# Kernel optimization log

Measured on AMD Instinct MI355X. Metric: run time of the kernel, lower is better.

The kernel has to match this reference:

```python
import jax, jax.numpy as jnp
import numpy as np

B, T, D = 8, 4096, 256
GATE_MIN, GATE_MAX = 0.01, 0.99


def setup_inputs() -> dict:
    key = jax.random.key(0)
    ks = jax.random.split(key, 8)
    inp = {
        "x_re": jax.random.normal(ks[0], (B, T, D), jnp.float32),
        "x_im": jax.random.normal(ks[1], (B, T, D), jnp.float32),
        "s0_re": jnp.zeros((B, D), jnp.float32),
        "s0_im": jnp.zeros((B, D), jnp.float32),
        "decay_re": jax.random.normal(ks[2], (D,), jnp.float32),
        "decay_im": 0.1 * jax.random.normal(ks[3], (D,), jnp.float32),
        "Wm": 0.02 * jax.random.normal(ks[4], (2 * D, 2 * D), jnp.float32)
              + jnp.eye(2 * D, dtype=jnp.float32),  # eye_ init on diag blocks
        "bm": jnp.zeros((2 * D,), jnp.float32),
        "Wo": 0.02 * jax.random.normal(ks[5], (2 * D, 2 * D), jnp.float32),
        "bo": jnp.zeros((2 * D,), jnp.float32),
        "Wg": 0.02 * jax.random.normal(ks[6], (D, 2 * D), jnp.float32),
        "bg": jnp.zeros((D,), jnp.float32),
    }
    return inp


def reference(x_re, x_im, s0_re, s0_im, decay_re, decay_im,
              Wm, bm, Wo, bo, Wg, bg):
    # decay = sigmoid(decay_re) + i*decay_im
    dr = jax.nn.sigmoid(decay_re)
    di = decay_im

    # scan over time: inputs as [T, B, D]
    xs = (jnp.swapaxes(x_re, 0, 1), jnp.swapaxes(x_im, 0, 1))

    def step(carry, xt):
        s_re, s_im = carry
        xr, xi = xt                                   # [B, D]
        x_cat = jnp.concatenate([xr, xi], axis=-1)    # [B, 2D]
        x_in = x_cat @ Wm.T + bm
        ur, ui = jnp.split(x_in, 2, axis=-1)
        # complex mul-add: new_state = prev_state * decay + update
        ns_re = s_re * dr - s_im * di + ur
        ns_im = s_re * di + s_im * dr + ui
        s_cat = jnp.concatenate([ns_re, ns_im], axis=-1)  # [B, 2D]
        source = s_cat @ Wo.T + bo                        # [B, 2D] (re|im)
        gate = jnp.clip(jax.nn.sigmoid(s_cat @ Wg.T + bg), GATE_MIN, GATE_MAX)
        y = jnp.concatenate([source, gate], axis=-1)      # [B, 3D]
        return (ns_re, ns_im), y

    _, ys = jax.lax.scan(step, (s0_re, s0_im), xs)        # [T, B, 3D]
    return jnp.swapaxes(ys, 0, 1)                          # [B, T, 3D] = [src_re|src_im|gate]
```

## Files before the change

kernel.cpp:

```cpp
#include <hip/hip_runtime.h>
#include <hip/hip_bf16.h>
#include <cstdint>
#include <cstddef>


typedef __bf16 bf16;
typedef __bf16 bf16x8 __attribute__((ext_vector_type(8)));
typedef float floatx4 __attribute__((ext_vector_type(4)));

#define NB 8
#define NT 4096
#define ND 256
#define BT (NB * NT)
#define TWOD 512
#define CHUNK 32
#define NCHUNK (NT / CHUNK)

static __device__ __forceinline__ float sigmoidf_(float x) {
  return 1.0f / (1.0f + __expf(-x));
}

static __device__ __forceinline__ void async_copy16(const void* g, void* l) {
  __builtin_amdgcn_global_load_lds(
      (__attribute__((address_space(1))) void*)g,
      (__attribute__((address_space(3))) void*)l, 16, 0, 0);
}

union U32BF2 { unsigned int u; __bf16 h[2]; };

__global__ void k_prep(const float* __restrict__ Wm,
                       const float* __restrict__ bm,
                       const float* __restrict__ Wo,
                       const float* __restrict__ Wg,
                       const float* __restrict__ bo,
                       const float* __restrict__ bg,
                       bf16* __restrict__ Wm_b,
                       bf16* __restrict__ Wc_b,
                       float* __restrict__ bm_p,
                       float* __restrict__ bc) {
  const int i = blockIdx.x * 256 + threadIdx.x;
  {
    const int r = i >> 9, c = i & 511;
    const int sr = (r >> 1) + (r & 1) * 256;
    Wm_b[i] = (bf16)Wm[sr * 512 + c];
  }
  {
    const int r = i >> 9, c = i & 511;
    const int sc = (c >> 1) + (c & 1) * 256;
    Wc_b[i] = (bf16)Wo[r * 512 + sc];
    if (i < 131072) Wc_b[262144 + i] = (bf16)Wg[r * 512 + sc];
  }
  if (i < 512) { bm_p[i] = bm[(i >> 1) + (i & 1) * 256]; bc[i] = bo[i]; }
  if (i < 256) bc[512 + i] = bg[i];
}

__global__ __launch_bounds__(256) void gemm1(
    const float* __restrict__ xre, const float* __restrict__ xim,
    const bf16* __restrict__ Bw, const float* __restrict__ bias,
    bf16* __restrict__ Cu,
    const float* __restrict__ decay_re, const float* __restrict__ decay_im,
    float* __restrict__ Fre, float* __restrict__ Fim) {
  __shared__ __align__(16) bf16 smem[128 * 128];
  bf16* As = smem;
  bf16* Bs = smem + 128 * 64;
  bf16* Us = smem;
  const int tid = threadIdx.x;
  const int wave = tid >> 6;
  const int lane = tid & 63;
  const int quad = lane >> 4;
  const int l16 = lane & 15;
  const int m0 = blockIdx.x * 128;
  const int n0 = blockIdx.y * 128;
  const int wm = (wave >> 1) * 64;
  const int wn = (wave & 1) * 64;
  const int srow = lane >> 3;
  const int schunk = (lane & 7) ^ (srow & 7);
  const int ar = tid >> 3;
  const int sg = tid & 7;

  floatx4 acc[4][4];
#pragma unroll
  for (int i = 0; i < 4; ++i)
#pragma unroll
    for (int j = 0; j < 4; ++j) acc[i][j] = (floatx4)0.0f;

  for (int k0 = 0; k0 < 512; k0 += 64) {
    const float* xs = (k0 < 256) ? xre : xim;
    const int xcol = k0 & 255;
    __syncthreads();
#pragma unroll
    for (int i = 0; i < 4; ++i) {
      const int seg = wave * 4 + i;
      const int row = seg * 8 + srow;
      async_copy16(Bw + (size_t)(n0 + row) * 512 + k0 + schunk * 8, Bs + seg * 512);
    }
#pragma unroll
    for (int it = 0; it < 4; ++it) {
      const int r = ar + 32 * it;
      const int cg = sg ^ (r & 7);
      const float* src = xs + (size_t)(m0 + r) * 256 + xcol + cg * 8;
      const float4 f0 = *(const float4*)(src);
      const float4 f1 = *(const float4*)(src + 4);
      bf16x8 v;
      v[0] = (bf16)f0.x; v[1] = (bf16)f0.y; v[2] = (bf16)f0.z; v[3] = (bf16)f0.w;
      v[4] = (bf16)f1.x; v[5] = (bf16)f1.y; v[6] = (bf16)f1.z; v[7] = (bf16)f1.w;
      *(bf16x8*)(As + r * 64 + sg * 8) = v;
    }
    __syncthreads();

#pragma unroll
    for (int s = 0; s < 2; ++s) {
      bf16x8 af[4], bfr[4];
#pragma unroll
      for (int mi = 0; mi < 4; ++mi) {
        const int row = wm + mi * 16 + l16;
        const int ch = ((s << 2) | quad) ^ (l16 & 7);
        af[mi] = *(const bf16x8*)(As + row * 64 + ch * 8);
      }
#pragma unroll
      for (int ni = 0; ni < 4; ++ni) {
        const int row = wn + ni * 16 + l16;
        const int ch = ((s << 2) | quad) ^ (l16 & 7);
        bfr[ni] = *(const bf16x8*)(Bs + row * 64 + ch * 8);
      }
#pragma unroll
      for (int mi = 0; mi < 4; ++mi)
#pragma unroll
        for (int ni = 0; ni < 4; ++ni)
          acc[mi][ni] = __builtin_amdgcn_mfma_f32_16x16x32_bf16(
              af[mi], bfr[ni], acc[mi][ni], 0, 0, 0);
    }
  }

  __syncthreads();
#pragma unroll
  for (int mi = 0; mi < 4; ++mi) {
    const int rloc = wm + mi * 16 + quad * 4;
#pragma unroll
    for (int ni = 0; ni < 4; ++ni) {
      const int cloc = wn + ni * 16 + l16;
      const float bb = bias[n0 + cloc];
#pragma unroll
      for (int r = 0; r < 4; ++r)
        Us[(rloc + r) * 128 + cloc] = (bf16)(acc[mi][ni][r] + bb);
    }
  }
  __syncthreads();
  {
    bf16* dst = Cu + (size_t)m0 * TWOD + n0;
#pragma unroll
    for (int i = 0; i < 8; ++i) {
      const int e = i * 256 + tid;
      const int row = e >> 4, ch = e & 15;
      *(bf16x8*)(dst + (size_t)row * TWOD + ch * 8) =
          *(const bf16x8*)(Us + row * 128 + ch * 8);
    }
  }
  {
    const int sc = tid >> 6;
    const int dd = tid & 63;
    const int d = (n0 >> 1) + dd;
    const float drr = sigmoidf_(decay_re[d]);
    const float dii = decay_im[d];
    float sr = 0.f, si = 0.f;
    const unsigned int* Up = (const unsigned int*)(Us + (sc * 32) * 128 + 2 * dd);
#pragma unroll 4
    for (int j = 0; j < 32; ++j) {
      U32BF2 cv; cv.u = Up[j * 64];
      const float ur = (float)cv.h[0];
      const float ui = (float)cv.h[1];
      const float nr = sr * drr - si * dii + ur;
      const float ni2 = sr * dii + si * drr + ui;
      sr = nr; si = ni2;
    }
    const int bidx = m0 >> 12;
    const int cchunk = ((m0 & 4095) >> 5) + sc;
    const int o = (bidx * NCHUNK + cchunk) * ND + d;
    Fre[o] = sr; Fim[o] = si;
  }
}

__global__ void k_scan2(const float* __restrict__ Fre,
                        const float* __restrict__ Fim,
                        const float* __restrict__ s0_re,
                        const float* __restrict__ s0_im,
                        const float* __restrict__ decay_re,
                        const float* __restrict__ decay_im,
                        float* __restrict__ Ire, float* __restrict__ Iim) {
  const int c = threadIdx.x;
  const int d = blockIdx.x;
  const int b = blockIdx.y;
  const float drr = sigmoidf_(decay_re[d]);
  const float dii = decay_im[d];
  float wr = drr, wi = dii;
#pragma unroll
  for (int i = 0; i < 5; ++i) {
    const float nr = wr * wr - wi * wi;
    const float ni = 2.f * wr * wi;
    wr = nr; wi = ni;
  }
  const int o = (b * NCHUNK + c) * ND + d;
  float vr = Fre[o], vi = Fim[o];
  float ar = 1.f, ai = 0.f;
  __shared__ float lr[128], li[128];
#pragma unroll
  for (int k = 1; k < 128; k <<= 1) {
    lr[c] = vr; li[c] = vi;
    __syncthreads();
    const float tr = (c >= k) ? lr[c - k] : 0.f;
    const float ti = (c >= k) ? li[c - k] : 0.f;
    __syncthreads();
    vr += wr * tr - wi * ti;
    vi += wr * ti + wi * tr;
    if (c & k) {
      const float nar = ar * wr - ai * wi;
      ai = ar * wi + ai * wr;
      ar = nar;
    }
    const float nwr = wr * wr - wi * wi;
    wi = 2.f * wr * wi;
    wr = nwr;
  }
  lr[c] = vr; li[c] = vi;
  __syncthreads();
  float er = (c > 0) ? lr[c - 1] : 0.f;
  float ei = (c > 0) ? li[c - 1] : 0.f;
  const float s0r = s0_re[b * ND + d];
  const float s0i = s0_im[b * ND + d];
  er += ar * s0r - ai * s0i;
  ei += ar * s0i + ai * s0r;
  Ire[o] = er; Iim[o] = ei;
}

__global__ void k_scan_pass3(bf16* __restrict__ U,
                             const float* __restrict__ decay_re,
                             const float* __restrict__ decay_im,
                             const float* __restrict__ Ire,
                             const float* __restrict__ Iim) {
  const int d = threadIdx.x;
  const int c = blockIdx.x;
  const int b = blockIdx.y;
  const float dr = sigmoidf_(decay_re[d]);
  const float di = decay_im[d];
  const int o = (b * NCHUNK + c) * ND + d;
  float sr = Ire[o], si = Iim[o];
  unsigned int* Ur = (unsigned int*)
      (U + ((size_t)b * NT + (size_t)c * CHUNK) * TWOD + 2 * d);
#pragma unroll 4
  for (int j = 0; j < CHUNK; ++j) {
    U32BF2 cv; cv.u = Ur[(size_t)j * (TWOD / 2)];
    const float ur = (float)cv.h[0];
    const float ui = (float)cv.h[1];
    const float nr = sr * dr - si * di + ur;
    const float ni = sr * di + si * dr + ui;
    sr = nr; si = ni;
    cv.h[0] = (bf16)nr; cv.h[1] = (bf16)ni;
    Ur[(size_t)j * (TWOD / 2)] = cv.u;
  }
}

__global__ __launch_bounds__(256) void gemm2(
    const bf16* __restrict__ A, const bf16* __restrict__ Bw,
    const float* __restrict__ bias, float* __restrict__ C) {
  __shared__ __align__(16) bf16 As[128 * 64];
  __shared__ __align__(16) bf16 Bs[64 * 64];
  const int tid = threadIdx.x;
  const int wave = tid >> 6;
  const int lane = tid & 63;
  const int quad = lane >> 4;
  const int l16 = lane & 15;
  const int m0 = blockIdx.x * 128;
  const int n0 = blockIdx.y * 64;
  const int wm = (wave >> 1) * 64;
  const int wn = (wave & 1) * 32;
  const int srow = lane >> 3;
  const int schunk = (lane & 7) ^ (srow & 7);

  floatx4 acc[4][2];
#pragma unroll
  for (int i = 0; i < 4; ++i)
#pragma unroll
    for (int j = 0; j < 2; ++j) acc[i][j] = (floatx4)0.0f;

  for (int k0 = 0; k0 < 512; k0 += 64) {
    __syncthreads();
#pragma unroll
    for (int i = 0; i < 4; ++i) {
      const int seg = wave * 4 + i;
      const int row = seg * 8 + srow;
      async_copy16(A + (size_t)(m0 + row) * 512 + k0 + schunk * 8, As + seg * 512);
    }
#pragma unroll
    for (int i = 0; i < 2; ++i) {
      const int seg = wave * 2 + i;
      const int row = seg * 8 + srow;
      async_copy16(Bw + (size_t)(n0 + row) * 512 + k0 + schunk * 8, Bs + seg * 512);
    }
    __syncthreads();

#pragma unroll
    for (int s = 0; s < 2; ++s) {
      bf16x8 af[4], bfr[2];
#pragma unroll
      for (int mi = 0; mi < 4; ++mi) {
        const int row = wm + mi * 16 + l16;
        const int ch = ((s << 2) | quad) ^ (l16 & 7);
        af[mi] = *(const bf16x8*)(As + row * 64 + ch * 8);
      }
#pragma unroll
      for (int ni = 0; ni < 2; ++ni) {
        const int row = wn + ni * 16 + l16;
        const int ch = ((s << 2) | quad) ^ (l16 & 7);
        bfr[ni] = *(const bf16x8*)(Bs + row * 64 + ch * 8);
      }
#pragma unroll
      for (int mi = 0; mi < 4; ++mi)
#pragma unroll
        for (int ni = 0; ni < 2; ++ni)
          acc[mi][ni] = __builtin_amdgcn_mfma_f32_16x16x32_bf16(
              af[mi], bfr[ni], acc[mi][ni], 0, 0, 0);
    }
  }

#pragma unroll
  for (int mi = 0; mi < 4; ++mi) {
    const int rb = m0 + wm + mi * 16 + quad * 4;
#pragma unroll
    for (int ni = 0; ni < 2; ++ni) {
      const int col = n0 + wn + ni * 16 + l16;
      const float bb = bias[col];
#pragma unroll
      for (int r = 0; r < 4; ++r) {
        float v = acc[mi][ni][r] + bb;
        if (col >= 512) v = fminf(fmaxf(sigmoidf_(v), 0.01f), 0.99f);
        C[(size_t)(rb + r) * 768 + col] = v;
      }
    }
  }
}


extern "C" void kernel_launch(void* const* d_in, const int* in_sizes, int n_in,
                              void* d_out, int out_size, void* d_ws, size_t ws_size,
                              hipStream_t stream) {
  const float* x_re = (const float*)d_in[0];
  const float* x_im = (const float*)d_in[1];
  const float* s0_re = (const float*)d_in[2];
  const float* s0_im = (const float*)d_in[3];
  const float* decay_re = (const float*)d_in[4];
  const float* decay_im = (const float*)d_in[5];
  const float* Wm = (const float*)d_in[6];
  const float* bm = (const float*)d_in[7];
  const float* Wo = (const float*)d_in[8];
  const float* bo = (const float*)d_in[9];
  const float* Wg = (const float*)d_in[10];
  const float* bg = (const float*)d_in[11];

  char* ws = (char*)d_ws;
  const size_t U_OFF = 0;
  const size_t WM_OFF = 33554432;
  const size_t WC_OFF = WM_OFF + 524288;
  const size_t BMP_OFF = WC_OFF + 786432;
  const size_t BC_OFF = BMP_OFF + 4096;
  const size_t FRE_OFF = BC_OFF + 4096;
  const size_t FIM_OFF = FRE_OFF + 1048576;
  const size_t IRE_OFF = FIM_OFF + 1048576;
  const size_t IIM_OFF = IRE_OFF + 1048576;

  bf16* U = (bf16*)(ws + U_OFF);
  bf16* Wm_b = (bf16*)(ws + WM_OFF);
  bf16* Wc_b = (bf16*)(ws + WC_OFF);
  float* bm_p = (float*)(ws + BMP_OFF);
  float* bc = (float*)(ws + BC_OFF);
  float* Fre = (float*)(ws + FRE_OFF);
  float* Fim = (float*)(ws + FIM_OFF);
  float* Ire = (float*)(ws + IRE_OFF);
  float* Iim = (float*)(ws + IIM_OFF);

  k_prep<<<dim3(1024), 256, 0, stream>>>(Wm, bm, Wo, Wg, bo, bg,
                                         Wm_b, Wc_b, bm_p, bc);
  gemm1<<<dim3(256, 4), 256, 0, stream>>>(x_re, x_im, Wm_b, bm_p, U,
                                          decay_re, decay_im, Fre, Fim);
  k_scan2<<<dim3(ND, NB), NCHUNK, 0, stream>>>(Fre, Fim, s0_re, s0_im,
                                               decay_re, decay_im, Ire, Iim);
  k_scan_pass3<<<dim3(NCHUNK, NB), ND, 0, stream>>>(U, decay_re, decay_im, Ire, Iim);
  gemm2<<<dim3(256, 12), 256, 0, stream>>>(U, Wc_b, bc, (float*)d_out);
}
```

Baseline: 253.6 us.

## Fuse chunk-carry fixup into gemm2 prologue, drop scan pass3 kernel

gemm1 now writes the local, chunk-relative scan states in fp32 instead of the bf16 projected input. gemm2 rebuilds the full state while loading A: it adds decay^(j+1) times the chunk carry-in, using a power table precomputed in k_prep, then converts to bf16 into LDS. This removes the separate pass3 kernel and its read-modify-write over U. In exchange the intermediate is fp32, twice the bytes, and gemm2 does extra loads and FMAs per element. gemm2's N tile also grows from 64 to 128, which halves the grid and reuses each A tile across more columns.

```diff
diff --git a/kernel.cpp b/kernel.cpp
--- a/kernel.cpp
+++ b/kernel.cpp
@@ -34,10 +34,13 @@
                        const float* __restrict__ Wg,
                        const float* __restrict__ bo,
                        const float* __restrict__ bg,
+                       const float* __restrict__ decay_re,
+                       const float* __restrict__ decay_im,
                        bf16* __restrict__ Wm_b,
                        bf16* __restrict__ Wc_b,
                        float* __restrict__ bm_p,
-                       float* __restrict__ bc) {
+                       float* __restrict__ bc,
+                       float* __restrict__ Ppow) {
   const int i = blockIdx.x * 256 + threadIdx.x;
   {
     const int r = i >> 9, c = i & 511;
@@ -52,12 +55,25 @@
   }
   if (i < 512) { bm_p[i] = bm[(i >> 1) + (i & 1) * 256]; bc[i] = bo[i]; }
   if (i < 256) bc[512 + i] = bg[i];
+  if (i < 8192) {
+    const int r = i >> 8, d = i & 255;
+    const float dr = sigmoidf_(decay_re[d]);
+    const float di = decay_im[d];
+    float wr = dr, wi = di;
+    for (int j = 0; j < r; ++j) {
+      const float nr = wr * dr - wi * di;
+      wi = wr * di + wi * dr;
+      wr = nr;
+    }
+    Ppow[2 * i] = wr;
+    Ppow[2 * i + 1] = wi;
+  }
 }
 
 __global__ __launch_bounds__(256) void gemm1(
     const float* __restrict__ xre, const float* __restrict__ xim,
     const bf16* __restrict__ Bw, const float* __restrict__ bias,
-    bf16* __restrict__ Cu,
+    float* __restrict__ Lf,
     const float* __restrict__ decay_re, const float* __restrict__ decay_im,
     float* __restrict__ Fre, float* __restrict__ Fim) {
   __shared__ __align__(16) bf16 smem[128 * 128];
@@ -147,16 +163,6 @@
   }
   __syncthreads();
   {
-    bf16* dst = Cu + (size_t)m0 * TWOD + n0;
-#pragma unroll
-    for (int i = 0; i < 8; ++i) {
-      const int e = i * 256 + tid;
-      const int row = e >> 4, ch = e & 15;
-      *(bf16x8*)(dst + (size_t)row * TWOD + ch * 8) =
-          *(const bf16x8*)(Us + row * 128 + ch * 8);
-    }
-  }
-  {
     const int sc = tid >> 6;
     const int dd = tid & 63;
     const int d = (n0 >> 1) + dd;
@@ -164,6 +170,7 @@
     const float dii = decay_im[d];
     float sr = 0.f, si = 0.f;
     const unsigned int* Up = (const unsigned int*)(Us + (sc * 32) * 128 + 2 * dd);
+    float2* Lp = (float2*)Lf + (size_t)(m0 + sc * 32) * 256 + d;
 #pragma unroll 4
     for (int j = 0; j < 32; ++j) {
       U32BF2 cv; cv.u = Up[j * 64];
@@ -172,6 +179,7 @@
       const float nr = sr * drr - si * dii + ur;
       const float ni2 = sr * dii + si * drr + ui;
       sr = nr; si = ni2;
+      Lp[(size_t)j * 256] = make_float2(nr, ni2);
     }
     const int bidx = m0 >> 12;
     const int cchunk = ((m0 & 4095) >> 5) + sc;
@@ -186,7 +194,7 @@
                         const float* __restrict__ s0_im,
                         const float* __restrict__ decay_re,
                         const float* __restrict__ decay_im,
-                        float* __restrict__ Ire, float* __restrict__ Iim) {
+                        float* __restrict__ Ic) {
   const int c = threadIdx.x;
   const int d = blockIdx.x;
   const int b = blockIdx.y;
@@ -229,58 +237,35 @@
   const float s0i = s0_im[b * ND + d];
   er += ar * s0r - ai * s0i;
   ei += ar * s0i + ai * s0r;
-  Ire[o] = er; Iim[o] = ei;
-}
-
-__global__ void k_scan_pass3(bf16* __restrict__ U,
-                             const float* __restrict__ decay_re,
-                             const float* __restrict__ decay_im,
-                             const float* __restrict__ Ire,
-                             const float* __restrict__ Iim) {
-  const int d = threadIdx.x;
-  const int c = blockIdx.x;
-  const int b = blockIdx.y;
-  const float dr = sigmoidf_(decay_re[d]);
-  const float di = decay_im[d];
-  const int o = (b * NCHUNK + c) * ND + d;
-  float sr = Ire[o], si = Iim[o];
-  unsigned int* Ur = (unsigned int*)
-      (U + ((size_t)b * NT + (size_t)c * CHUNK) * TWOD + 2 * d);
-#pragma unroll 4
-  for (int j = 0; j < CHUNK; ++j) {
-    U32BF2 cv; cv.u = Ur[(size_t)j * (TWOD / 2)];
-    const float ur = (float)cv.h[0];
-    const float ui = (float)cv.h[1];
-    const float nr = sr * dr - si * di + ur;
-    const float ni = sr * di + si * dr + ui;
-    sr = nr; si = ni;
-    cv.h[0] = (bf16)nr; cv.h[1] = (bf16)ni;
-    Ur[(size_t)j * (TWOD / 2)] = cv.u;
-  }
+  ((float2*)Ic)[o] = make_float2(er, ei);
 }
 
 __global__ __launch_bounds__(256) void gemm2(
-    const bf16* __restrict__ A, const bf16* __restrict__ Bw,
-    const float* __restrict__ bias, float* __restrict__ C) {
+    const float* __restrict__ Lf, const bf16* __restrict__ Bw,
+    const float* __restrict__ bias, const float* __restrict__ Ppow,
+    const float* __restrict__ Ic, float* __restrict__ C) {
   __shared__ __align__(16) bf16 As[128 * 64];
-  __shared__ __align__(16) bf16 Bs[64 * 64];
+  __shared__ __align__(16) bf16 Bs[128 * 64];
   const int tid = threadIdx.x;
   const int wave = tid >> 6;
   const int lane = tid & 63;
   const int quad = lane >> 4;
   const int l16 = lane & 15;
   const int m0 = blockIdx.x * 128;
-  const int n0 = blockIdx.y * 64;
+  const int n0 = blockIdx.y * 128;
   const int wm = (wave >> 1) * 64;
-  const int wn = (wave & 1) * 32;
+  const int wn = (wave & 1) * 64;
   const int srow = lane >> 3;
   const int schunk = (lane & 7) ^ (srow & 7);
-
-  floatx4 acc[4][2];
+  const int ar = tid >> 3;
+  const int sg = tid & 7;
+  const int cb0 = (m0 >> 12) * NCHUNK + ((m0 & 4095) >> 5);
+
+  floatx4 acc[4][4];
 #pragma unroll
   for (int i = 0; i < 4; ++i)
 #pragma unroll
-    for (int j = 0; j < 2; ++j) acc[i][j] = (floatx4)0.0f;
+    for (int j = 0; j < 4; ++j) acc[i][j] = (floatx4)0.0f;
 
   for (int k0 = 0; k0 < 512; k0 += 64) {
     __syncthreads();
@@ -288,19 +273,37 @@
     for (int i = 0; i < 4; ++i) {
       const int seg = wave * 4 + i;
       const int row = seg * 8 + srow;
-      async_copy16(A + (size_t)(m0 + row) * 512 + k0 + schunk * 8, As + seg * 512);
-    }
-#pragma unroll
-    for (int i = 0; i < 2; ++i) {
-      const int seg = wave * 2 + i;
-      const int row = seg * 8 + srow;
       async_copy16(Bw + (size_t)(n0 + row) * 512 + k0 + schunk * 8, Bs + seg * 512);
     }
+#pragma unroll
+    for (int it = 0; it < 4; ++it) {
+      const int r = ar + 32 * it;
+      const int cg = sg ^ (r & 7);
+      const int db = (k0 >> 1) + cg * 4;
+      const float* src = Lf + (size_t)(m0 + r) * 512 + k0 + cg * 8;
+      const float4 f0 = *(const float4*)(src);
+      const float4 f1 = *(const float4*)(src + 4);
+      const float4* pwp = (const float4*)(Ppow + 2 * ((size_t)((r & 31) * 256) + db));
+      const float4 p0 = pwp[0], p1 = pwp[1];
+      const int c = cb0 + (r >> 5);
+      const float4* icp = (const float4*)(Ic + 2 * ((size_t)c * 256 + db));
+      const float4 i0 = icp[0], i1 = icp[1];
+      bf16x8 v;
+      v[0] = (bf16)(f0.x + p0.x * i0.x - p0.y * i0.y);
+      v[1] = (bf16)(f0.y + p0.x * i0.y + p0.y * i0.x);
+      v[2] = (bf16)(f0.z + p0.z * i0.z - p0.w * i0.w);
+      v[3] = (bf16)(f0.w + p0.z * i0.w + p0.w * i0.z);
+      v[4] = (bf16)(f1.x + p1.x * i1.x - p1.y * i1.y);
+      v[5] = (bf16)(f1.y + p1.x * i1.y + p1.y * i1.x);
+      v[6] = (bf16)(f1.z + p1.z * i1.z - p1.w * i1.w);
+      v[7] = (bf16)(f1.w + p1.z * i1.w + p1.w * i1.z);
+      *(bf16x8*)(As + r * 64 + sg * 8) = v;
+    }
     __syncthreads();
 
 #pragma unroll
     for (int s = 0; s < 2; ++s) {
-      bf16x8 af[4], bfr[2];
+      bf16x8 af[4], bfr[4];
 #pragma unroll
       for (int mi = 0; mi < 4; ++mi) {
         const int row = wm + mi * 16 + l16;
@@ -308,7 +311,7 @@
         af[mi] = *(const bf16x8*)(As + row * 64 + ch * 8);
       }
 #pragma unroll
-      for (int ni = 0; ni < 2; ++ni) {
+      for (int ni = 0; ni < 4; ++ni) {
         const int row = wn + ni * 16 + l16;
         const int ch = ((s << 2) | quad) ^ (l16 & 7);
         bfr[ni] = *(const bf16x8*)(Bs + row * 64 + ch * 8);
@@ -316,7 +319,7 @@
 #pragma unroll
       for (int mi = 0; mi < 4; ++mi)
 #pragma unroll
-        for (int ni = 0; ni < 2; ++ni)
+        for (int ni = 0; ni < 4; ++ni)
           acc[mi][ni] = __builtin_amdgcn_mfma_f32_16x16x32_bf16(
               af[mi], bfr[ni], acc[mi][ni], 0, 0, 0);
     }
@@ -326,7 +329,7 @@
   for (int mi = 0; mi < 4; ++mi) {
     const int rb = m0 + wm + mi * 16 + quad * 4;
 #pragma unroll
-    for (int ni = 0; ni < 2; ++ni) {
+    for (int ni = 0; ni < 4; ++ni) {
       const int col = n0 + wn + ni * 16 + l16;
       const float bb = bias[col];
 #pragma unroll
@@ -357,32 +360,32 @@
   const float* bg = (const float*)d_in[11];
 
   char* ws = (char*)d_ws;
-  const size_t U_OFF = 0;
-  const size_t WM_OFF = 33554432;
+  const size_t L_OFF = 0;
+  const size_t WM_OFF = 67108864;
   const size_t WC_OFF = WM_OFF + 524288;
   const size_t BMP_OFF = WC_OFF + 786432;
   const size_t BC_OFF = BMP_OFF + 4096;
   const size_t FRE_OFF = BC_OFF + 4096;
   const size_t FIM_OFF = FRE_OFF + 1048576;
-  const size_t IRE_OFF = FIM_OFF + 1048576;
-  const size_t IIM_OFF = IRE_OFF + 1048576;
-
-  bf16* U = (bf16*)(ws + U_OFF);
+  const size_t IC_OFF = FIM_OFF + 1048576;
+  const size_t PPOW_OFF = IC_OFF + 2097152;
+
+  float* Lf = (float*)(ws + L_OFF);
   bf16* Wm_b = (bf16*)(ws + WM_OFF);
   bf16* Wc_b = (bf16*)(ws + WC_OFF);
   float* bm_p = (float*)(ws + BMP_OFF);
   float* bc = (float*)(ws + BC_OFF);
   float* Fre = (float*)(ws + FRE_OFF);
   float* Fim = (float*)(ws + FIM_OFF);
-  float* Ire = (float*)(ws + IRE_OFF);
-  float* Iim = (float*)(ws + IIM_OFF);
+  float* Ic = (float*)(ws + IC_OFF);
+  float* Ppow = (float*)(ws + PPOW_OFF);
 
   k_prep<<<dim3(1024), 256, 0, stream>>>(Wm, bm, Wo, Wg, bo, bg,
-                                         Wm_b, Wc_b, bm_p, bc);
-  gemm1<<<dim3(256, 4), 256, 0, stream>>>(x_re, x_im, Wm_b, bm_p, U,
+                                         decay_re, decay_im,
+                                         Wm_b, Wc_b, bm_p, bc, Ppow);
+  gemm1<<<dim3(256, 4), 256, 0, stream>>>(x_re, x_im, Wm_b, bm_p, Lf,
                                           decay_re, decay_im, Fre, Fim);
   k_scan2<<<dim3(ND, NB), NCHUNK, 0, stream>>>(Fre, Fim, s0_re, s0_im,
-                                               decay_re, decay_im, Ire, Iim);
-  k_scan_pass3<<<dim3(NCHUNK, NB), ND, 0, stream>>>(U, decay_re, decay_im, Ire, Iim);
-  gemm2<<<dim3(256, 12), 256, 0, stream>>>(U, Wc_b, bc, (float*)d_out);
-}
+                                               decay_re, decay_im, Ic);
+  gemm2<<<dim3(256, 6), 256, 0, stream>>>(Lf, Wc_b, bc, Ppow, Ic, (float*)d_out);
+}
```

After: 272.9 us. +7.6%, slower.
